# Performance work log

Measured on AMD Instinct MI355X. Metric: run time of the kernel, lower is better.

## Reference

```python
import jax, jax.numpy as jnp
import numpy as np

B, S, D, H = 4, 2048, 1024, 16
HD = D // H
SCALE = HD ** -0.5


def setup_inputs() -> dict:
    key = jax.random.key(0)
    ks = jax.random.split(key, 5)
    std = D ** -0.5
    return {
        "x": jax.random.normal(ks[0], (B, S, D), jnp.float32),
        "wq": jax.random.normal(ks[1], (D, D), jnp.float32) * std,
        "bq": jnp.zeros((D,), jnp.float32),
        "wk": jax.random.normal(ks[2], (D, D), jnp.float32) * std,
        "bk": jnp.zeros((D,), jnp.float32),
        "wv": jax.random.normal(ks[3], (D, D), jnp.float32) * std,
        "bv": jnp.zeros((D,), jnp.float32),
        "wo": jax.random.normal(ks[4], (D, D), jnp.float32) * std,
        "bo": jnp.zeros((D,), jnp.float32),
    }


def reference(x, wq, bq, wk, bk, wv, bv, wo, bo):
    # projections; weights stored as [in, out] so y = x @ w + b
    q = (x @ wq + bq).reshape(B, S, H, HD).transpose(0, 2, 1, 3)  # [B,H,S,HD]
    k = (x @ wk + bk).reshape(B, S, H, HD).transpose(0, 2, 1, 3)
    v = (x @ wv + bv).reshape(B, S, H, HD).transpose(0, 2, 1, 3)
    attn = jnp.einsum("bhqd,bhkd->bhqk", q, k) * SCALE  # [B,H,S,S]
    attn = jax.nn.softmax(attn, axis=-1)
    out = jnp.einsum("bhqk,bhkd->bhqd", attn, v)  # [B,H,S,HD]
    out = out.transpose(0, 2, 1, 3).reshape(B, S, D)
    return out @ wo + bo
```

## Files before the change

kernel.cpp:

```cpp
#include <hip/hip_runtime.h>
#include <stdint.h>


typedef __attribute__((ext_vector_type(8))) short bf16x8;
typedef __attribute__((ext_vector_type(4))) short bf16x4;
typedef __attribute__((ext_vector_type(4))) float f32x4;
typedef __attribute__((ext_vector_type(16))) float f32x16;
typedef __attribute__((ext_vector_type(4))) int i32x4;
typedef unsigned short u16;
typedef unsigned int u32;

#define AS1 __attribute__((address_space(1)))
#define AS3 __attribute__((address_space(3)))

#define SCALE_L2E 0.18033688011112042f

__device__ __forceinline__ void gld_lds16(const void* g, void* l) {
  __builtin_amdgcn_global_load_lds((const AS1 void*)g, (AS3 void*)l, 16, 0, 0);
}

__device__ __forceinline__ u16 f2bf(float f) {
  u32 x = __builtin_bit_cast(u32, f);
  x += 0x7fff + ((x >> 16) & 1);
  return (u16)(x >> 16);
}

__device__ __forceinline__ u16 f2bf_fast(float a) {
#if __has_builtin(__builtin_amdgcn_cvt_pk_bf16_f32)
  auto v = __builtin_amdgcn_cvt_pk_bf16_f32(a, a);
  return (u16)(__builtin_bit_cast(u32, v) & 0xffffu);
#else
  return f2bf(a);
#endif
}

__device__ __forceinline__ u32 pk2(float a, float b) {
#if __has_builtin(__builtin_amdgcn_cvt_pk_bf16_f32)
  return __builtin_bit_cast(u32, __builtin_amdgcn_cvt_pk_bf16_f32(a, b));
#else
  return (u32)f2bf(a) | ((u32)f2bf(b) << 16);
#endif
}

__device__ __forceinline__ float exp2_fast(float x) {
#if __has_builtin(__builtin_amdgcn_exp2f)
  return __builtin_amdgcn_exp2f(x);
#else
  return exp2f(x);
#endif
}

__device__ __forceinline__ f32x16 zero16() {
  f32x16 z;
#pragma unroll
  for (int i = 0; i < 16; ++i) z[i] = 0.f;
  return z;
}

__global__ __launch_bounds__(256) void convert_x(const float* __restrict__ x,
                                                 u16* __restrict__ xb) {
  int i = (blockIdx.x * 256 + threadIdx.x) * 4;
  float4 v = *(const float4*)(x + i);
  ushort4 o;
  o.x = f2bf(v.x); o.y = f2bf(v.y); o.z = f2bf(v.z); o.w = f2bf(v.w);
  *(ushort4*)(xb + i) = o;
}

__global__ __launch_bounds__(256) void pack_weights(
    const float* __restrict__ wq, const float* __restrict__ wk,
    const float* __restrict__ wv, const float* __restrict__ wo,
    u16* __restrict__ wt_qkv, u16* __restrict__ wt_o) {
  __shared__ float tile[64][65];
  int mat = blockIdx.z;
  const float* src = (mat == 0) ? wq : (mat == 1) ? wk : (mat == 2) ? wv : wo;
  int k0 = blockIdx.y * 64, j0 = blockIdx.x * 64;
  int t = threadIdx.x;
  int lr = t >> 6;
  int lc = t & 63;
#pragma unroll
  for (int it = 0; it < 16; ++it) {
    int r = it * 4 + lr;
    tile[r][lc] = src[(size_t)(k0 + r) * 1024 + j0 + lc];
  }
  __syncthreads();
  u16* dst = (mat == 3) ? wt_o : (wt_qkv + (size_t)mat * 1024 * 1024);
#pragma unroll
  for (int it = 0; it < 16; ++it) {
    int nl = it * 4 + lr;
    float v = tile[lc][nl];
    if (mat == 0) v *= SCALE_L2E;
    dst[(size_t)(j0 + nl) * 1024 + k0 + lc] = f2bf(v);
  }
}

__global__ __launch_bounds__(512, 2) void gemm256_qkv(
    const u16* __restrict__ A, const u16* __restrict__ Bt,
    const float* __restrict__ bias0, const float* __restrict__ bias1,
    const float* __restrict__ bias2,
    u16* __restrict__ outQ, u16* __restrict__ outK, u16* __restrict__ outV) {
  __shared__ u16 lA[2][256 * 64];
  __shared__ u16 lB[2][256 * 64];
  int tid = threadIdx.x;
  int wave = tid >> 6, lane = tid & 63;
  int wr = wave >> 2, wc = wave & 3;

  int bid = blockIdx.x;
  int xcd = bid & 7, j = bid >> 3;
  int m0 = (xcd * 4 + (j & 3)) * 256;
  int n0 = (j >> 2) * 256;

  f32x4 acc[8][4];
#pragma unroll
  for (int fm = 0; fm < 8; ++fm)
#pragma unroll
    for (int fn = 0; fn < 4; ++fn) acc[fm][fn] = f32x4{0.f, 0.f, 0.f, 0.f};

  int srow = lane >> 3;
  int scol = (lane & 7) * 8;
  int fr = lane & 15;
  int kq = (lane >> 4) * 8;

#pragma unroll
  for (int seg = 0; seg < 4; ++seg) {
    int r0 = seg * 64 + wave * 8;
    gld_lds16(A + (size_t)(m0 + r0 + srow) * 1024 + scol, &lA[0][r0 * 64]);
    gld_lds16(Bt + (size_t)(n0 + r0 + srow) * 1024 + scol, &lB[0][r0 * 64]);
  }
  __syncthreads();

  int cur = 0;
  for (int kt = 0; kt < 16; ++kt) {
    if (kt < 15) {
      int k1 = (kt + 1) * 64;
#pragma unroll
      for (int seg = 0; seg < 4; ++seg) {
        int r0 = seg * 64 + wave * 8;
        gld_lds16(A + (size_t)(m0 + r0 + srow) * 1024 + k1 + scol,
                  &lA[cur ^ 1][r0 * 64]);
        gld_lds16(Bt + (size_t)(n0 + r0 + srow) * 1024 + k1 + scol,
                  &lB[cur ^ 1][r0 * 64]);
      }
    }
    const u16* la = lA[cur];
    const u16* lb = lB[cur];
#pragma unroll
    for (int ks = 0; ks < 2; ++ks) {
      bf16x8 af[8], bfv[4];
#pragma unroll
      for (int fm = 0; fm < 8; ++fm)
        af[fm] = *(const bf16x8*)(la + (wr * 128 + fm * 16 + fr) * 64 + ks * 32 + kq);
#pragma unroll
      for (int fn = 0; fn < 4; ++fn)
        bfv[fn] = *(const bf16x8*)(lb + (wc * 64 + fn * 16 + fr) * 64 + ks * 32 + kq);
#pragma unroll
      for (int fm = 0; fm < 8; ++fm)
#pragma unroll
        for (int fn = 0; fn < 4; ++fn)
          acc[fm][fn] = __builtin_amdgcn_mfma_f32_16x16x32_bf16(
              af[fm], bfv[fn], acc[fm][fn], 0, 0, 0);
    }
    __syncthreads();
    cur ^= 1;
  }

  int mat = n0 >> 10;
  const float* bp = (mat == 0) ? bias0 : (mat == 1) ? bias1 : bias2;
  int rb0 = m0 + wr * 128 + (lane >> 4) * 4;
  int jb = (n0 & 1023) + wc * 64;
#pragma unroll
  for (int fn = 0; fn < 4; ++fn) {
    int jj = jb + fn * 16 + fr;
    float bv = bp[jj];
    if (mat == 0) bv *= SCALE_L2E;
    if (mat == 2) {
      int h = jj >> 6, hd = jj & 63;
#pragma unroll
      for (int fm = 0; fm < 8; ++fm) {
        int row0 = rb0 + fm * 16;
        int b = row0 >> 11, s = row0 & 2047;
        int ci = s >> 6, sl = s & 63;
        int slice = sl >> 4, srem = sl & 15;
        size_t off = (size_t)(b * 16 + h) * 131072 + ci * 4096 + slice * 1024
                   + ((srem >> 2) & 1) * 512 + hd * 8 + (srem >> 3) * 4;
        ushort4 pk;
        pk.x = f2bf_fast(acc[fm][fn][0] + bv);
        pk.y = f2bf_fast(acc[fm][fn][1] + bv);
        pk.z = f2bf_fast(acc[fm][fn][2] + bv);
        pk.w = f2bf_fast(acc[fm][fn][3] + bv);
        *(ushort4*)(outV + off) = pk;
      }
    } else {
      u16* base = (mat == 0) ? outQ : outK;
#pragma unroll
      for (int fm = 0; fm < 8; ++fm)
#pragma unroll
        for (int rr = 0; rr < 4; ++rr)
          base[(size_t)(rb0 + fm * 16 + rr) * 1024 + jj] =
              f2bf_fast(acc[fm][fn][rr] + bv);
    }
  }
}

template <int MODE>
__global__ __launch_bounds__(256, 3) void gemm_bt(
    const u16* __restrict__ A, const u16* __restrict__ Bt,
    const float* __restrict__ bias0, const float* __restrict__ bias1,
    const float* __restrict__ bias2,
    void* __restrict__ out0v, void* __restrict__ out1v, void* __restrict__ out2v) {
  __shared__ u16 lA[128 * 32];
  __shared__ u16 lB[128 * 32];
  const int K = 1024;
  int tid = threadIdx.x;
  int wave = tid >> 6, lane = tid & 63;

  int bid = blockIdx.x;
  int n0 = (bid & 7) * 128;
  int m0 = (bid >> 3) * 128;
  int wm = (wave & 1) * 64, wn = (wave >> 1) * 64;

  f32x4 acc[4][4];
#pragma unroll
  for (int i = 0; i < 4; ++i)
#pragma unroll
    for (int jj = 0; jj < 4; ++jj) acc[i][jj] = f32x4{0.f, 0.f, 0.f, 0.f};

  int srow = lane >> 2;
  int scol = (lane & 3) * 8;

  for (int k0 = 0; k0 < K; k0 += 32) {
#pragma unroll
    for (int c = 0; c < 2; ++c) {
      int rbase = wave * 32 + c * 16;
      gld_lds16(A + (size_t)(m0 + rbase + srow) * K + k0 + scol, lA + rbase * 32);
      gld_lds16(Bt + (size_t)(n0 + rbase + srow) * K + k0 + scol, lB + rbase * 32);
    }
    __syncthreads();
    bf16x8 af[4], bfr[4];
#pragma unroll
    for (int mt = 0; mt < 4; ++mt)
      af[mt] = *(const bf16x8*)(lA + (wm + mt * 16 + (lane & 15)) * 32 + (lane >> 4) * 8);
#pragma unroll
    for (int nt = 0; nt < 4; ++nt)
      bfr[nt] = *(const bf16x8*)(lB + (wn + nt * 16 + (lane & 15)) * 32 + (lane >> 4) * 8);
#pragma unroll
    for (int mt = 0; mt < 4; ++mt)
#pragma unroll
      for (int nt = 0; nt < 4; ++nt)
        acc[mt][nt] = __builtin_amdgcn_mfma_f32_16x16x32_bf16(af[mt], bfr[nt], acc[mt][nt], 0, 0, 0);
    __syncthreads();
  }

  int rbase0 = m0 + wm + (lane >> 4) * 4;
  int cbase = n0 + wn + (lane & 15);
#pragma unroll
  for (int nt = 0; nt < 4; ++nt) {
    int col = cbase + nt * 16;
    float bv = bias0[col];
    float* o = (float*)out0v;
#pragma unroll
    for (int mt = 0; mt < 4; ++mt)
#pragma unroll
      for (int r = 0; r < 4; ++r) {
        int row = rbase0 + mt * 16 + r;
        o[(size_t)row * 1024 + col] = acc[mt][nt][r] + bv;
      }
  }
}

__global__ __launch_bounds__(512, 2) void flash_attn(
    const u16* __restrict__ Q, const u16* __restrict__ Kb,
    const u16* __restrict__ Vg, u16* __restrict__ ctx) {
  __shared__ u16 lK[2][64 * 32];
  __shared__ u16 lV[4096];
  int tid = threadIdx.x, wave = tid >> 6, lane = tid & 63;

  int F = blockIdx.x;
  int xcd = F & 7, idx = F >> 3;
  int bh = xcd * 8 + (idx >> 2);
  int q0 = (idx & 3) * 512;
  int b = bh >> 4, h = bh & 15;
  const u16* Qp = Q + (size_t)b * 2048 * 1024 + h * 64;
  const u16* Kp = Kb + (size_t)b * 2048 * 1024 + h * 64;
  const u16* Vp = Vg + (size_t)bh * 131072;

  int ql = lane & 31;
  int hi = lane >> 5;

  bf16x8 qf[2][4];
#pragma unroll
  for (int qt = 0; qt < 2; ++qt) {
    const u16* qrow = Qp + (size_t)(q0 + wave * 64 + qt * 32 + ql) * 1024;
#pragma unroll
    for (int kk = 0; kk < 4; ++kk)
      qf[qt][kk] = *(const bf16x8*)(qrow + kk * 16 + hi * 8);
  }

  float lsum[2] = {0.f, 0.f};
  f32x16 o[2][2];
#pragma unroll
  for (int qt = 0; qt < 2; ++qt)
#pragma unroll
    for (int dh = 0; dh < 2; ++dh) o[qt][dh] = zero16();

  int srow = lane >> 2;
  int schunk = (((lane & 3) ^ ((lane >> 3) & 3)) * 8);
  int kk_w = wave & 1;
  int rb = wave >> 1;
  int stg_row = rb * 16 + srow;
  int rkey = ((lane & 15) >> 1) & 3;

  const u16* gK = Kp + (size_t)stg_row * 1024 + kk_w * 32 + schunk;
  const u16* gV = Vp + wave * 512 + lane * 8;
  u16* wK = lK[kk_w] + rb * 512 + lane * 8;
  u16* wV = lV + wave * 512 + lane * 8;

  i32x4 ldK = *(const i32x4*)gK;
  i32x4 ldV = *(const i32x4*)gV;
  *(i32x4*)wK = ldK;
  *(i32x4*)wV = ldV;
  __syncthreads();

  for (int s0 = 0; s0 < 2048; s0 += 64) {
    bool more = (s0 + 64 < 2048);
    if (more) {
      ldK = *(const i32x4*)(gK + (size_t)(s0 + 64) * 1024);
      ldV = *(const i32x4*)(gV + (size_t)(s0 + 64) * 64);
    }

#pragma unroll
    for (int sb = 0; sb < 2; ++sb) {
      bf16x8 kf[4];
      int krb = (sb * 32 + ql) * 32;
#pragma unroll
      for (int kk = 0; kk < 4; ++kk)
        kf[kk] = *(const bf16x8*)(lK[kk >> 1] + krb + ((((kk & 1) << 1) | hi) ^ rkey) * 8);

      f32x16 sa0 = zero16(), sa1 = zero16();
#pragma unroll
      for (int kk = 0; kk < 4; ++kk) {
        sa0 = __builtin_amdgcn_mfma_f32_32x32x16_bf16(kf[kk], qf[0][kk], sa0, 0, 0, 0);
        sa1 = __builtin_amdgcn_mfma_f32_32x32x16_bf16(kf[kk], qf[1][kk], sa1, 0, 0, 0);
      }

      bf16x8 pu[2][2];
#pragma unroll
      for (int qt = 0; qt < 2; ++qt) {
        float p[16];
#pragma unroll
        for (int r = 0; r < 16; ++r)
          p[r] = exp2_fast(qt == 0 ? sa0[r] : sa1[r]);
        float a0 = (p[0] + p[1]) + (p[2] + p[3]);
        float a1 = (p[4] + p[5]) + (p[6] + p[7]);
        float a2 = (p[8] + p[9]) + (p[10] + p[11]);
        float a3 = (p[12] + p[13]) + (p[14] + p[15]);
        lsum[qt] += (a0 + a1) + (a2 + a3);
#pragma unroll
        for (int ss = 0; ss < 2; ++ss) {
          union { u32 w[4]; bf16x8 v; } pk_;
          pk_.w[0] = pk2(p[8 * ss + 0], p[8 * ss + 1]);
          pk_.w[1] = pk2(p[8 * ss + 2], p[8 * ss + 3]);
          pk_.w[2] = pk2(p[8 * ss + 4], p[8 * ss + 5]);
          pk_.w[3] = pk2(p[8 * ss + 6], p[8 * ss + 7]);
          pu[qt][ss] = pk_.v;
        }
      }

#pragma unroll
      for (int ss = 0; ss < 2; ++ss) {
        int vbase = (sb * 2 + ss) * 1024 + hi * 512 + ql * 8;
#pragma unroll
        for (int dh = 0; dh < 2; ++dh) {
          bf16x8 vf = *(const bf16x8*)(lV + vbase + dh * 256);
          o[0][dh] = __builtin_amdgcn_mfma_f32_32x32x16_bf16(vf, pu[0][ss], o[0][dh], 0, 0, 0);
          o[1][dh] = __builtin_amdgcn_mfma_f32_32x32x16_bf16(vf, pu[1][ss], o[1][dh], 0, 0, 0);
        }
      }
    }

    __syncthreads();
    if (more) {
      *(i32x4*)wK = ldK;
      *(i32x4*)wV = ldV;
    }
    __syncthreads();
  }

#pragma unroll
  for (int qt = 0; qt < 2; ++qt) {
    float rs = lsum[qt] + __shfl_xor(lsum[qt], 32);
    float inv = 1.0f / fmaxf(rs, 1e-30f);
    int q = q0 + wave * 64 + qt * 32 + ql;
    size_t rowbase = ((size_t)(b * 2048 + q) * 16 + h) * 64;
#pragma unroll
    for (int dh = 0; dh < 2; ++dh)
#pragma unroll
      for (int rr = 0; rr < 4; ++rr) {
        ushort4 pk;
        pk.x = f2bf_fast(o[qt][dh][4 * rr + 0] * inv);
        pk.y = f2bf_fast(o[qt][dh][4 * rr + 1] * inv);
        pk.z = f2bf_fast(o[qt][dh][4 * rr + 2] * inv);
        pk.w = f2bf_fast(o[qt][dh][4 * rr + 3] * inv);
        *(ushort4*)(ctx + rowbase + dh * 32 + rr * 8 + hi * 4) = pk;
      }
  }
}

extern "C" void kernel_launch(void* const* d_in, const int* in_sizes, int n_in,
                              void* d_out, int out_size, void* d_ws, size_t ws_size,
                              hipStream_t stream) {
  const float* x  = (const float*)d_in[0];
  const float* wq = (const float*)d_in[1];
  const float* bq = (const float*)d_in[2];
  const float* wk = (const float*)d_in[3];
  const float* bk = (const float*)d_in[4];
  const float* wv = (const float*)d_in[5];
  const float* bv = (const float*)d_in[6];
  const float* wo = (const float*)d_in[7];
  const float* bo = (const float*)d_in[8];

  u16* ws = (u16*)d_ws;
  u16* xb     = ws;
  u16* wt_qkv = xb + (size_t)8192 * 1024;
  u16* wt_o   = wt_qkv + (size_t)3072 * 1024;
  u16* Qb     = wt_o + (size_t)1024 * 1024;
  u16* Kbuf   = Qb + (size_t)8192 * 1024;
  u16* Vgb    = Kbuf + (size_t)8192 * 1024;
  u16* ctx    = Vgb + (size_t)8192 * 1024;

  convert_x<<<8192, 256, 0, stream>>>(x, xb);
  pack_weights<<<dim3(16, 16, 4), 256, 0, stream>>>(wq, wk, wv, wo, wt_qkv, wt_o);
  gemm256_qkv<<<384, 512, 0, stream>>>(xb, wt_qkv, bq, bk, bv, Qb, Kbuf, Vgb);
  flash_attn<<<256, 512, 0, stream>>>(Qb, Kbuf, Vgb, ctx);
  gemm_bt<1><<<512, 256, 0, stream>>>(ctx, wt_o, bo, nullptr, nullptr,
                                      d_out, nullptr, nullptr);
}
```

Before: 306.4 us.

## Shrink QKV GEMM tile to 128x256x32 with swizzled LDS and higher occupancy

Replaces the 256x256 QKV projection tile (K-step 64) with a 128x256 tile and K-step 32, launching 768 blocks instead of 384 and raising launch bounds to four blocks per CU. LDS loads and reads use an XOR swizzle on the 16-byte chunk index to avoid bank conflicts. The goal is better CU fill and latency hiding from more resident blocks and smaller per-block LDS and register use. The cost is less data reuse per tile, more global traffic for the B operand, and twice as many barrier-separated K iterations.

```diff
diff --git a/kernel.cpp b/kernel.cpp
--- a/kernel.cpp
+++ b/kernel.cpp
@@ -93,79 +93,70 @@
   }
 }
 
-__global__ __launch_bounds__(512, 2) void gemm256_qkv(
+__global__ __launch_bounds__(512, 4) void gemm_qkv(
     const u16* __restrict__ A, const u16* __restrict__ Bt,
     const float* __restrict__ bias0, const float* __restrict__ bias1,
     const float* __restrict__ bias2,
     u16* __restrict__ outQ, u16* __restrict__ outK, u16* __restrict__ outV) {
-  __shared__ u16 lA[2][256 * 64];
-  __shared__ u16 lB[2][256 * 64];
+  __shared__ u16 lA[2][128 * 32];
+  __shared__ u16 lB[2][256 * 32];
   int tid = threadIdx.x;
   int wave = tid >> 6, lane = tid & 63;
   int wr = wave >> 2, wc = wave & 3;
 
   int bid = blockIdx.x;
   int xcd = bid & 7, j = bid >> 3;
-  int m0 = (xcd * 4 + (j & 3)) * 256;
-  int n0 = (j >> 2) * 256;
-
-  f32x4 acc[8][4];
-#pragma unroll
-  for (int fm = 0; fm < 8; ++fm)
+  int m0 = (xcd * 8 + (j & 7)) * 128;
+  int n0 = (j >> 3) * 256;
+
+  f32x4 acc[4][4];
+#pragma unroll
+  for (int fm = 0; fm < 4; ++fm)
 #pragma unroll
     for (int fn = 0; fn < 4; ++fn) acc[fm][fn] = f32x4{0.f, 0.f, 0.f, 0.f};
 
-  int srow = lane >> 3;
-  int scol = (lane & 7) * 8;
+  int srow = lane >> 2;
+  int schunk = ((lane & 3) ^ ((lane >> 3) & 3)) * 8;
   int fr = lane & 15;
-  int kq = (lane >> 4) * 8;
-
-#pragma unroll
-  for (int seg = 0; seg < 4; ++seg) {
-    int r0 = seg * 64 + wave * 8;
-    gld_lds16(A + (size_t)(m0 + r0 + srow) * 1024 + scol, &lA[0][r0 * 64]);
-    gld_lds16(Bt + (size_t)(n0 + r0 + srow) * 1024 + scol, &lB[0][r0 * 64]);
-  }
+  int rpos = (((lane >> 4) ^ ((fr >> 1) & 3))) * 8;
+
+  const u16* Asrc = A + (size_t)(m0 + wave * 16 + srow) * 1024 + schunk;
+  const u16* Bsrc0 = Bt + (size_t)(n0 + wave * 32 + srow) * 1024 + schunk;
+  const u16* Bsrc1 = Bsrc0 + (size_t)16 * 1024;
+
+  gld_lds16(Asrc, &lA[0][wave * 16 * 32]);
+  gld_lds16(Bsrc0, &lB[0][wave * 32 * 32]);
+  gld_lds16(Bsrc1, &lB[0][(wave * 32 + 16) * 32]);
   __syncthreads();
 
   int cur = 0;
-  for (int kt = 0; kt < 16; ++kt) {
-    if (kt < 15) {
-      int k1 = (kt + 1) * 64;
-#pragma unroll
-      for (int seg = 0; seg < 4; ++seg) {
-        int r0 = seg * 64 + wave * 8;
-        gld_lds16(A + (size_t)(m0 + r0 + srow) * 1024 + k1 + scol,
-                  &lA[cur ^ 1][r0 * 64]);
-        gld_lds16(Bt + (size_t)(n0 + r0 + srow) * 1024 + k1 + scol,
-                  &lB[cur ^ 1][r0 * 64]);
-      }
-    }
-    const u16* la = lA[cur];
-    const u16* lb = lB[cur];
-#pragma unroll
-    for (int ks = 0; ks < 2; ++ks) {
-      bf16x8 af[8], bfv[4];
-#pragma unroll
-      for (int fm = 0; fm < 8; ++fm)
-        af[fm] = *(const bf16x8*)(la + (wr * 128 + fm * 16 + fr) * 64 + ks * 32 + kq);
+  for (int kt = 0; kt < 32; ++kt) {
+    if (kt < 31) {
+      int k1 = (kt + 1) * 32;
+      gld_lds16(Asrc + k1, &lA[cur ^ 1][wave * 16 * 32]);
+      gld_lds16(Bsrc0 + k1, &lB[cur ^ 1][wave * 32 * 32]);
+      gld_lds16(Bsrc1 + k1, &lB[cur ^ 1][(wave * 32 + 16) * 32]);
+    }
+    bf16x8 af[4], bfv[4];
+#pragma unroll
+    for (int fm = 0; fm < 4; ++fm)
+      af[fm] = *(const bf16x8*)(&lA[cur][(wr * 64 + fm * 16 + fr) * 32 + rpos]);
+#pragma unroll
+    for (int fn = 0; fn < 4; ++fn)
+      bfv[fn] = *(const bf16x8*)(&lB[cur][(wc * 64 + fn * 16 + fr) * 32 + rpos]);
+#pragma unroll
+    for (int fm = 0; fm < 4; ++fm)
 #pragma unroll
       for (int fn = 0; fn < 4; ++fn)
-        bfv[fn] = *(const bf16x8*)(lb + (wc * 64 + fn * 16 + fr) * 64 + ks * 32 + kq);
-#pragma unroll
-      for (int fm = 0; fm < 8; ++fm)
-#pragma unroll
-        for (int fn = 0; fn < 4; ++fn)
-          acc[fm][fn] = __builtin_amdgcn_mfma_f32_16x16x32_bf16(
-              af[fm], bfv[fn], acc[fm][fn], 0, 0, 0);
-    }
+        acc[fm][fn] = __builtin_amdgcn_mfma_f32_16x16x32_bf16(
+            af[fm], bfv[fn], acc[fm][fn], 0, 0, 0);
     __syncthreads();
     cur ^= 1;
   }
 
   int mat = n0 >> 10;
   const float* bp = (mat == 0) ? bias0 : (mat == 1) ? bias1 : bias2;
-  int rb0 = m0 + wr * 128 + (lane >> 4) * 4;
+  int rb0 = m0 + wr * 64 + (lane >> 4) * 4;
   int jb = (n0 & 1023) + wc * 64;
 #pragma unroll
   for (int fn = 0; fn < 4; ++fn) {
@@ -175,7 +166,7 @@
     if (mat == 2) {
       int h = jj >> 6, hd = jj & 63;
 #pragma unroll
-      for (int fm = 0; fm < 8; ++fm) {
+      for (int fm = 0; fm < 4; ++fm) {
         int row0 = rb0 + fm * 16;
         int b = row0 >> 11, s = row0 & 2047;
         int ci = s >> 6, sl = s & 63;
@@ -192,7 +183,7 @@
     } else {
       u16* base = (mat == 0) ? outQ : outK;
 #pragma unroll
-      for (int fm = 0; fm < 8; ++fm)
+      for (int fm = 0; fm < 4; ++fm)
 #pragma unroll
         for (int rr = 0; rr < 4; ++rr)
           base[(size_t)(rb0 + fm * 16 + rr) * 1024 + jj] =
@@ -429,7 +420,7 @@
 
   convert_x<<<8192, 256, 0, stream>>>(x, xb);
   pack_weights<<<dim3(16, 16, 4), 256, 0, stream>>>(wq, wk, wv, wo, wt_qkv, wt_o);
-  gemm256_qkv<<<384, 512, 0, stream>>>(xb, wt_qkv, bq, bk, bv, Qb, Kbuf, Vgb);
+  gemm_qkv<<<768, 512, 0, stream>>>(xb, wt_qkv, bq, bk, bv, Qb, Kbuf, Vgb);
   flash_attn<<<256, 512, 0, stream>>>(Qb, Kbuf, Vgb, ctx);
   gemm_bt<1><<<512, 256, 0, stream>>>(ctx, wt_o, bo, nullptr, nullptr,
                                       d_out, nullptr, nullptr);
```

Measured after the change: 279.7 us. -8.7%, faster.
